# Performance work log

Hardware: AMD Instinct MI355X
Metric: run time of the kernel (lower is better)

The kernel has to match this reference:

```python
import jax, jax.numpy as jnp
import numpy as np

B, C_IN, C_OUT = 16, 256, 128
V_RAW, N_VERT, K = 10242, 40962, 7


def setup_inputs() -> dict:
    key = jax.random.key(0)
    k1, k2, k3, k4, k5, k6 = jax.random.split(key, 6)
    x = jax.random.normal(k1, (B, C_IN, V_RAW), dtype=jnp.float32)
    W = jax.random.normal(k2, (C_OUT, C_IN), dtype=jnp.float32) * (1.0 / np.sqrt(C_IN))
    b = jax.random.normal(k3, (C_OUT,), dtype=jnp.float32) * 0.01
    up_neigh_indices = jax.random.randint(k4, (N_VERT, K), 0, N_VERT, dtype=jnp.int64)
    down_indices = jax.random.randint(k5, (V_RAW,), 0, N_VERT, dtype=jnp.int64)
    max_pool_indices = jax.random.randint(k6, (B, C_OUT, V_RAW), 0, K, dtype=jnp.int64)
    return {"x": x, "W": W, "b": b,
            "up_neigh_indices": up_neigh_indices,
            "down_indices": down_indices,
            "max_pool_indices": max_pool_indices}


def _feats_indices(n_feats: int, n_raw_vertices: int) -> np.ndarray:
    # torch: floor(linspace(0, n_feats, num=n_raw_vertices*n_feats)); last -= 1
    fi = np.floor(np.linspace(0.0, float(n_feats), num=n_raw_vertices * n_feats))
    fi[-1] -= 1
    return fi.astype(np.int64)


def reference(x, W, b, up_neigh_indices, down_indices, max_pool_indices):
    n_samples, in_feats, n_raw = x.shape
    n_vertices = up_neigh_indices.shape[0]
    out_feats = W.shape[0]

    # per-vertex linear projection: (B, Cin, V) -> (B, Cout, V)
    h = jnp.einsum('bcv,oc->bov', x, W) + b[None, :, None]

    # neighbor table at coarse vertices: (V_raw, K)
    neigh = up_neigh_indices[down_indices]

    # vertices_indices[b, f, v] = neigh[v, max_pool_indices[b, f, v]]
    vi = neigh[jnp.arange(n_raw)[None, None, :], max_pool_indices]  # (B, Cout, V_raw)

    # flatten exactly like torch (row-major over (Cout, V_raw))
    h_flat = h.reshape(n_samples, out_feats * n_raw)
    vi_flat = vi.reshape(n_samples, out_feats * n_raw)
    fi = jnp.asarray(_feats_indices(out_feats, n_raw))  # (Cout*V_raw,) static

    y = jnp.zeros((n_samples, out_feats, n_vertices), dtype=h.dtype)
    y = y.at[jnp.arange(n_samples)[:, None], fi[None, :], vi_flat].set(h_flat)
    return y
```

## Files before the change

### kernel.cpp

```cpp
#include <hip/hip_runtime.h>

#define NB    16
#define CIN   256
#define COUT  128
#define VRAW  10242
#define NVERT 40962
#define HALF  20481

typedef __attribute__((ext_vector_type(8))) short short8;
typedef __attribute__((ext_vector_type(4))) float floatx4;

__device__ inline unsigned short f2bf(float f) {
    unsigned u = __builtin_bit_cast(unsigned, f);
    u += 0x7fffu + ((u >> 16) & 1u);
    return (unsigned short)(u >> 16);
}

__global__ __launch_bounds__(256) void convw_kernel(const float* __restrict__ W,
                                                    unsigned short* __restrict__ Wbf) {
    int i = blockIdx.x * 256 + threadIdx.x;
    Wbf[i] = f2bf(W[i]);
}

__global__ __launch_bounds__(256) void gemm_kernel(const float* __restrict__ x,
                                                   const unsigned short* __restrict__ Wbf,
                                                   const float* __restrict__ bias,
                                                   float* __restrict__ h) {
    const int b    = blockIdx.y;
    const int v0   = blockIdx.x * 128;
    const int wave = threadIdx.x >> 6;
    const int lane = threadIdx.x & 63;
    const int mn   = lane & 15;
    const int q    = lane >> 4;

    const int vw = v0 + wave * 32;

    floatx4 acc[8][2];
#pragma unroll
    for (int ot = 0; ot < 8; ot++) { acc[ot][0] = (floatx4)0.f; acc[ot][1] = (floatx4)0.f; }

#pragma unroll
    for (int ck = 0; ck < 8; ck++) {
        const int c0 = ck * 32;
        short8 bfrag[2];
#pragma unroll
        for (int vt = 0; vt < 2; vt++) {
            const int v   = vw + vt * 16 + mn;
            const bool ok = v < VRAW;
            const float* xp = x + ((size_t)b * CIN + (c0 + q * 8)) * VRAW + v;
#pragma unroll
            for (int j = 0; j < 8; j++) {
                float xv = ok ? xp[(size_t)j * VRAW] : 0.f;
                bfrag[vt][j] = (short)f2bf(xv);
            }
        }
#pragma unroll
        for (int ot = 0; ot < 8; ot++) {
            short8 afrag = *(const short8*)(Wbf + (ot * 16 + mn) * CIN + c0 + q * 8);
            acc[ot][0] = __builtin_amdgcn_mfma_f32_16x16x32_bf16(afrag, bfrag[0], acc[ot][0], 0, 0, 0);
            acc[ot][1] = __builtin_amdgcn_mfma_f32_16x16x32_bf16(afrag, bfrag[1], acc[ot][1], 0, 0, 0);
        }
    }

#pragma unroll
    for (int ot = 0; ot < 8; ot++) {
#pragma unroll
        for (int vt = 0; vt < 2; vt++) {
            const int v = vw + vt * 16 + mn;
            if (v < VRAW) {
#pragma unroll
                for (int r = 0; r < 4; r++) {
                    const int o = ot * 16 + q * 4 + r;
                    h[((size_t)b * COUT + o) * VRAW + v] = acc[ot][vt][r] + bias[o];
                }
            }
        }
    }
}

__global__ __launch_bounds__(1024) void scatter_kernel(const int* __restrict__ up,
                                                       const int* __restrict__ down,
                                                       const int* __restrict__ mpi,
                                                       const float* __restrict__ h,
                                                       float* __restrict__ y) {
    __shared__ unsigned st[(HALF + 1) / 2];
    const int r     = blockIdx.x >> 1;
    const int tbase = (blockIdx.x & 1) * HALF;
    const int tid   = threadIdx.x;

    for (int i = tid; i < (HALF + 1) / 2; i += 1024) st[i] = 0u;
    __syncthreads();

    const int* mpiRow = mpi + (size_t)r * VRAW;
    for (int v = tid; v < VRAW; v += 1024) {
        const int k = mpiRow[v];
        const int t = up[down[v] * 7 + k];
        const unsigned lt = (unsigned)(t - tbase);
        if (lt < (unsigned)HALF) {
            const unsigned val = (unsigned)(v + 1);
            const unsigned sh  = (lt & 1u) * 16u;
            unsigned* p = &st[lt >> 1];
            unsigned old = *p;
            while (true) {
                unsigned cur = (old >> sh) & 0xffffu;
                if (cur >= val) break;
                unsigned nw = (old & ~(0xffffu << sh)) | (val << sh);
                unsigned prev = atomicCAS(p, old, nw);
                if (prev == old) break;
                old = prev;
            }
        }
    }
    __syncthreads();

    const float* hRow = h + (size_t)r * VRAW;
    float* yRow = y + (size_t)r * NVERT + tbase;
    for (int lt = tid; lt < HALF; lt += 1024) {
        const unsigned s = (st[(unsigned)lt >> 1] >> (((unsigned)lt & 1u) * 16u)) & 0xffffu;
        yRow[lt] = s ? hRow[s - 1] : 0.0f;
    }
}

extern "C" void kernel_launch(void* const* d_in, const int* in_sizes, int n_in,
                              void* d_out, int out_size, void* d_ws, size_t ws_size,
                              hipStream_t stream) {
    const float* x    = (const float*)d_in[0];
    const float* W    = (const float*)d_in[1];
    const float* bias = (const float*)d_in[2];
    const int*   up   = (const int*)d_in[3];
    const int*   down = (const int*)d_in[4];
    const int*   mpi  = (const int*)d_in[5];
    float* y = (float*)d_out;

    unsigned short* Wbf = (unsigned short*)d_ws;
    float* h = (float*)((char*)d_ws + 65536);

    convw_kernel<<<COUT * CIN / 256, 256, 0, stream>>>(W, Wbf);

    dim3 ggrid((VRAW + 127) / 128, NB);
    gemm_kernel<<<ggrid, 256, 0, stream>>>(x, Wbf, bias, h);

    scatter_kernel<<<NB * COUT * 2, 1024, 0, stream>>>(up, down, mpi, h, y);
}
```

Before: 815.9 us.

## Replace atomic LDS scatter with inverted-bucket gather and stage GEMM inputs in LDS

Adds a build kernel that inverts the (vertex, neighbour slot) to target mapping into fixed-capacity buckets per target vertex. The output pass then becomes a per-row gather: each thread picks the largest matching source vertex for its target, which replaces the shared-memory CAS max loop and the split of each row into two halves. The GEMM now loads x tiles cooperatively into LDS as bf16 with vectorized reads before building the MFMA fragments, instead of each lane doing strided global loads. The cost is an extra memset and build kernel each call, and a CAP of 16 entries per bucket that silently drops contributions if a target receives more sources than that.

```diff
diff --git a/kernel.cpp b/kernel.cpp
--- a/kernel.cpp
+++ b/kernel.cpp
@@ -5,9 +5,12 @@
 #define COUT  128
 #define VRAW  10242
 #define NVERT 40962
-#define HALF  20481
+#define NPAIR (VRAW * 7)
+#define CAP   16
+#define LDV   132
 
 typedef __attribute__((ext_vector_type(8))) short short8;
+typedef __attribute__((ext_vector_type(4))) short short4v;
 typedef __attribute__((ext_vector_type(4))) float floatx4;
 
 __device__ inline unsigned short f2bf(float f) {
@@ -22,37 +25,78 @@
     Wbf[i] = f2bf(W[i]);
 }
 
+__global__ __launch_bounds__(256) void build_kernel(const int* __restrict__ up,
+                                                    const int* __restrict__ down,
+                                                    int* __restrict__ cnt,
+                                                    unsigned* __restrict__ buckets) {
+    int i = blockIdx.x * 256 + threadIdx.x;
+    if (i >= NPAIR) return;
+    int v = i / 7;
+    int k = i - v * 7;
+    int t = up[down[v] * 7 + k];
+    int pos = atomicAdd(&cnt[t], 1);
+    if (pos < CAP) buckets[(size_t)pos * NVERT + t] = ((unsigned)v << 3) | (unsigned)k;
+}
+
 __global__ __launch_bounds__(256) void gemm_kernel(const float* __restrict__ x,
                                                    const unsigned short* __restrict__ Wbf,
                                                    const float* __restrict__ bias,
                                                    float* __restrict__ h) {
+    __shared__ unsigned short xs[32 * LDV];
     const int b    = blockIdx.y;
     const int v0   = blockIdx.x * 128;
-    const int wave = threadIdx.x >> 6;
-    const int lane = threadIdx.x & 63;
+    const int tid  = threadIdx.x;
+    const int wave = tid >> 6;
+    const int lane = tid & 63;
     const int mn   = lane & 15;
     const int q    = lane >> 4;
+    const int vw   = wave * 32;
 
-    const int vw = v0 + wave * 32;
+    const int sc = tid >> 4;
+    const int sv = (tid & 15) * 8;
+    const bool fullTile = (v0 + 128 <= VRAW);
 
     floatx4 acc[8][2];
 #pragma unroll
     for (int ot = 0; ot < 8; ot++) { acc[ot][0] = (floatx4)0.f; acc[ot][1] = (floatx4)0.f; }
 
-#pragma unroll
     for (int ck = 0; ck < 8; ck++) {
         const int c0 = ck * 32;
+        __syncthreads();
+#pragma unroll
+        for (int p = 0; p < 2; p++) {
+            const int c = p * 16 + sc;
+            const float* src = x + ((size_t)(b * CIN + c0 + c)) * VRAW + v0 + sv;
+            float f[8];
+            if (fullTile) {
+#pragma unroll
+                for (int u = 0; u < 4; u++) {
+                    float2 tt = *(const float2*)(src + 2 * u);
+                    f[2 * u] = tt.x; f[2 * u + 1] = tt.y;
+                }
+            } else {
+#pragma unroll
+                for (int u = 0; u < 8; u++) {
+                    int v = v0 + sv + u;
+                    f[u] = (v < VRAW) ? src[u] : 0.f;
+                }
+            }
+            short4v lo, hi;
+#pragma unroll
+            for (int u = 0; u < 4; u++) { lo[u] = (short)f2bf(f[u]); hi[u] = (short)f2bf(f[4 + u]); }
+            unsigned short* dst = &xs[c * LDV + sv];
+            *(short4v*)dst = lo;
+            *(short4v*)(dst + 4) = hi;
+        }
+        __syncthreads();
+
         short8 bfrag[2];
 #pragma unroll
         for (int vt = 0; vt < 2; vt++) {
-            const int v   = vw + vt * 16 + mn;
-            const bool ok = v < VRAW;
-            const float* xp = x + ((size_t)b * CIN + (c0 + q * 8)) * VRAW + v;
+            const int vloc = vw + vt * 16 + mn;
 #pragma unroll
-            for (int j = 0; j < 8; j++) {
-                float xv = ok ? xp[(size_t)j * VRAW] : 0.f;
-                bfrag[vt][j] = (short)f2bf(xv);
-            }
+            for (int j = 0; j < 8; j++)
+                bfrag[vt][j] = (short)xs[(q * 8 + j) * LDV + vloc];
         }
 #pragma unroll
         for (int ot = 0; ot < 8; ot++) {
@@ -66,7 +110,7 @@
     for (int ot = 0; ot < 8; ot++) {
 #pragma unroll
         for (int vt = 0; vt < 2; vt++) {
-            const int v = vw + vt * 16 + mn;
+            const int v = v0 + vw + vt * 16 + mn;
             if (v < VRAW) {
 #pragma unroll
                 for (int r = 0; r < 4; r++) {
@@ -78,46 +122,36 @@
     }
 }
 
-__global__ __launch_bounds__(1024) void scatter_kernel(const int* __restrict__ up,
-                                                       const int* __restrict__ down,
-                                                       const int* __restrict__ mpi,
-                                                       const float* __restrict__ h,
-                                                       float* __restrict__ y) {
-    __shared__ unsigned st[(HALF + 1) / 2];
-    const int r     = blockIdx.x >> 1;
-    const int tbase = (blockIdx.x & 1) * HALF;
-    const int tid   = threadIdx.x;
+__global__ __launch_bounds__(1024) void gather_kernel(const int* __restrict__ cnt,
+                                                      const unsigned* __restrict__ buckets,
+                                                      const int* __restrict__ mpi,
+                                                      const float* __restrict__ h,
+                                                      float* __restrict__ y) {
+    __shared__ unsigned short mpis[VRAW];
+    __shared__ float hs[VRAW];
+    const int r   = blockIdx.x;
+    const int tid = threadIdx.x;
 
-    for (int i = tid; i < (HALF + 1) / 2; i += 1024) st[i] = 0u;
-    __syncthreads();
-
-    const int* mpiRow = mpi + (size_t)r * VRAW;
-    for (int v = tid; v < VRAW; v += 1024) {
-        const int k = mpiRow[v];
-        const int t = up[down[v] * 7 + k];
-        const unsigned lt = (unsigned)(t - tbase);
-        if (lt < (unsigned)HALF) {
-            const unsigned val = (unsigned)(v + 1);
-            const unsigned sh  = (lt & 1u) * 16u;
-            unsigned* p = &st[lt >> 1];
-            unsigned old = *p;
-            while (true) {
-                unsigned cur = (old >> sh) & 0xffffu;
-                if (cur >= val) break;
-                unsigned nw = (old & ~(0xffffu << sh)) | (val << sh);
-                unsigned prev = atomicCAS(p, old, nw);
-                if (prev == old) break;
-                old = prev;
-            }
-        }
+    const int*   mpiRow = mpi + (size_t)r * VRAW;
+    const float* hRow   = h   + (size_t)r * VRAW;
+    for (int i = tid; i < VRAW; i += 1024) {
+        mpis[i] = (unsigned short)mpiRow[i];
+        hs[i]   = hRow[i];
     }
     __syncthreads();
 
-    const float* hRow = h + (size_t)r * VRAW;
-    float* yRow = y + (size_t)r * NVERT + tbase;
-    for (int lt = tid; lt < HALF; lt += 1024) {
-        const unsigned s = (st[(unsigned)lt >> 1] >> (((unsigned)lt & 1u) * 16u)) & 0xffffu;
-        yRow[lt] = s ? hRow[s - 1] : 0.0f;
+    float* yRow = y + (size_t)r * NVERT;
+    for (int t = tid; t < NVERT; t += 1024) {
+        int n = cnt[t];
+        if (n > CAP) n = CAP;
+        int best = -1;
+        for (int j = 0; j < n; j++) {
+            const unsigned e = buckets[(size_t)j * NVERT + t];
+            const int v = (int)(e >> 3);
+            const int k = (int)(e & 7u);
+            if ((int)mpis[v] == k && v > best) best = v;
+        }
+        yRow[t] = (best >= 0) ? hs[best] : 0.0f;
     }
 }
 
@@ -132,13 +166,19 @@
     const int*   mpi  = (const int*)d_in[5];
     float* y = (float*)d_out;
 
-    unsigned short* Wbf = (unsigned short*)d_ws;
-    float* h = (float*)((char*)d_ws + 65536);
+    char* ws = (char*)d_ws;
+    unsigned short* Wbf = (unsigned short*)ws;
+    int*      cnt     = (int*)(ws + 65536);
+    unsigned* buckets = (unsigned*)(ws + 65536 + 163904);
+    float*    h       = (float*)(ws + 65536 + 163904 + (size_t)CAP * NVERT * 4);
 
     convw_kernel<<<COUT * CIN / 256, 256, 0, stream>>>(W, Wbf);
+
+    hipMemsetAsync(cnt, 0, NVERT * sizeof(int), stream);
+    build_kernel<<<(NPAIR + 255) / 256, 256, 0, stream>>>(up, down, cnt, buckets);
 
     dim3 ggrid((VRAW + 127) / 128, NB);
     gemm_kernel<<<ggrid, 256, 0, stream>>>(x, Wbf, bias, h);
 
-    scatter_kernel<<<NB * COUT * 2, 1024, 0, stream>>>(up, down, mpi, h, y);
+    gather_kernel<<<NB * COUT, 1024, 0, stream>>>(cnt, buckets, mpi, h, y);
 }
```

Result: no change. 816.1 us (+0.0%).
